# Kernel optimization log

Measured on AMD Instinct MI355X. Metric: run time of the kernel, lower is better.

Reference implementation:

```python
import jax, jax.numpy as jnp
import numpy as np

SEQ, D, N = 8192, 1024, 4096

def setup_inputs() -> dict:
    key = jax.random.key(0)
    kx, kw, kb = jax.random.split(key, 3)
    x = jax.random.normal(kx, (SEQ, D), dtype=jnp.float32)
    W = jax.random.normal(kw, (N, D), dtype=jnp.float32) * (1.0 / np.sqrt(D))
    b = jax.random.normal(kb, (N,), dtype=jnp.float32) * 0.01
    return {"x": x, "W": W, "b": b}

def reference(x, W, b):
    # Each NEURON computes tanh(w . e + b_i); stacking over neurons and
    # over the embedding list is a single fused matmul + bias + activation.
    # out: [seq, numNeurons]
    return jnp.tanh(jnp.einsum('sd,nd->sn', x, W) + b)
```

## Files before the change

kernel.cpp:

```cpp
#include <hip/hip_runtime.h>
#include <hip/hip_fp16.h>

#define SEQ 8192
#define DIM 1024
#define NN  4096
#define NT  16
#define A_BYTES ((size_t)SEQ * DIM * 2)
#define B_BYTES ((size_t)NN * DIM * 2)

using f16x8 = __attribute__((ext_vector_type(8))) _Float16;
using f16x4 = __attribute__((ext_vector_type(4))) _Float16;
using f32x4 = __attribute__((ext_vector_type(4))) float;

typedef __attribute__((address_space(1))) unsigned char as1_u8;
typedef __attribute__((address_space(3))) unsigned char as3_u8;

__device__ __forceinline__ float fast_tanh(float x) {
    float e = __expf(2.0f * x);
    return 1.0f - 2.0f / (e + 1.0f);
}

__global__ __launch_bounds__(256) void convert_kernel(
        const float* __restrict__ x, const float* __restrict__ w,
        f16x4* __restrict__ A, f16x4* __restrict__ B) {
    const int tid = threadIdx.x;
    const int b   = blockIdx.x;
    if (b < 8192) {
        const int gid = b * 256 + tid;
        const int s   = gid >> 8;
        const int c   = gid & 255;
        const float4 v = ((const float4*)x)[(size_t)s * 256 + c];
        const float f[4] = {v.x, v.y, v.z, v.w};
        f16x4 hv;
#pragma unroll
        for (int e = 0; e < 4; e++) hv[e] = (_Float16)f[e];
        A[(size_t)s * 256 + c] = hv;
    } else {
        const int gid = (b - 8192) * 256 + tid;
        const int n   = gid >> 8;
        const int c   = gid & 255;
        const float4 v = ((const float4*)w)[(size_t)n * 256 + c];
        const float f[4] = {v.x, v.y, v.z, v.w};
        f16x4 hv;
#pragma unroll
        for (int e = 0; e < 4; e++) hv[e] = (_Float16)f[e];
        B[(size_t)n * 256 + c] = hv;
    }
}

__global__ __launch_bounds__(512, 1) void gemm_tanh_kernel(
        const _Float16* __restrict__ A,
        const _Float16* __restrict__ B,
        const float* __restrict__ bias,
        float* __restrict__ out) {
    __shared__ _Float16 lds[65536];

    const int tid  = threadIdx.x;
    const int lane = tid & 63;
    const int wave = tid >> 6;
    const int wm   = wave >> 2;
    const int wn   = wave & 3;
    const int l15  = lane & 15;
    const int lq   = lane >> 4;

    const int wgid = ((blockIdx.x & 7) << 6) | (blockIdx.x >> 3);
    const int qb = wgid >> 5;
    const int pb = wgid & 31;
    const int rowBase = pb << 8;
    const int colBase = qb << 8;

    const int sw  = l15 & 7;
    const int gk0 = ((lq)     ^ sw) << 4;
    const int gk1 = ((4 + lq) ^ sw) << 4;
    const int aOff = wm * 2048 + l15 * 128;
    const int bOff = 32768 + wn * 2048 + l15 * 128;

    const int srow = tid >> 3;
    const int sg   = (tid & 7) ^ (srow & 7);
    const unsigned ldsWave = (unsigned)wave << 10;

    const _Float16* Ag = A + (size_t)(rowBase + srow) * DIM + sg * 8;
    const _Float16* Bg = B + (size_t)(colBase + srow) * DIM + sg * 8;
    char* ldsc = (char*)lds;

    auto stageA = [&](int kt, int h, int d) {
        const _Float16* g = Ag + (size_t)h * 128 * DIM + kt * 64;
        const unsigned lo = (unsigned)d * 65536u + (unsigned)h * 16384u + ldsWave;
        __builtin_amdgcn_global_load_lds((const as1_u8*)g,
                                         (as3_u8*)(ldsc + lo), 16, 0, 0);
        __builtin_amdgcn_global_load_lds((const as1_u8*)(g + (size_t)64 * DIM),
                                         (as3_u8*)(ldsc + lo + 8192), 16, 0, 0);
    };
    auto stageB = [&](int kt, int h, int d) {
        const _Float16* g = Bg + (size_t)h * 128 * DIM + kt * 64;
        const unsigned lo = (unsigned)d * 65536u + 32768u + (unsigned)h * 16384u + ldsWave;
        __builtin_amdgcn_global_load_lds((const as1_u8*)g,
                                         (as3_u8*)(ldsc + lo), 16, 0, 0);
        __builtin_amdgcn_global_load_lds((const as1_u8*)(g + (size_t)64 * DIM),
                                         (as3_u8*)(ldsc + lo + 8192), 16, 0, 0);
    };

    f32x4 acc[8][4] = {};
    f16x8 aH0[4][2], aH1[4][2], bN01[2][2], bN23[2][2];

    stageA(0, 0, 0); stageA(0, 1, 0); stageB(0, 0, 0); stageB(0, 1, 0);
    asm volatile("s_waitcnt vmcnt(0)" ::: "memory");
    __builtin_amdgcn_sched_barrier(0);
    __builtin_amdgcn_s_barrier();
    __builtin_amdgcn_sched_barrier(0);
#pragma unroll
    for (int i = 0; i < 4; ++i) {
        aH0[i][0] = *(const f16x8*)(ldsc + aOff + i * 4096 + gk0);
        aH0[i][1] = *(const f16x8*)(ldsc + aOff + i * 4096 + gk1);
    }
#pragma unroll
    for (int j = 0; j < 2; ++j) {
        bN01[j][0] = *(const f16x8*)(ldsc + bOff + j * 8192 + gk0);
        bN01[j][1] = *(const f16x8*)(ldsc + bOff + j * 8192 + gk1);
    }

    for (int t = 0; t < NT; ++t) {
        const int d  = t & 1;
        const int dn = d ^ 1;
        const char* lb  = ldsc + d * 65536;
        const char* lbn = ldsc + dn * 65536;

        if (t + 1 < NT) {
            stageA(t + 1, 0, dn); stageA(t + 1, 1, dn);
            stageB(t + 1, 0, dn); stageB(t + 1, 1, dn);
        }

#pragma unroll
        for (int j = 0; j < 2; ++j) {
            bN23[j][0] = *(const f16x8*)(lb + bOff + 16384 + j * 8192 + gk0);
            bN23[j][1] = *(const f16x8*)(lb + bOff + 16384 + j * 8192 + gk1);
        }
        __builtin_amdgcn_s_setprio(1);
#pragma unroll
        for (int k = 0; k < 2; ++k)
#pragma unroll
            for (int i = 0; i < 4; ++i)
#pragma unroll
                for (int j = 0; j < 2; ++j)
                    acc[i][j] = __builtin_amdgcn_mfma_f32_16x16x32_f16(
                        aH0[i][k], bN01[j][k], acc[i][j], 0, 0, 0);
        __builtin_amdgcn_s_setprio(0);

#pragma unroll
        for (int i = 0; i < 4; ++i) {
            aH1[i][0] = *(const f16x8*)(lb + aOff + 16384 + i * 4096 + gk0);
            aH1[i][1] = *(const f16x8*)(lb + aOff + 16384 + i * 4096 + gk1);
        }
        __builtin_amdgcn_s_setprio(1);
#pragma unroll
        for (int k = 0; k < 2; ++k)
#pragma unroll
            for (int i = 0; i < 4; ++i)
#pragma unroll
                for (int j = 0; j < 2; ++j)
                    acc[i][2 + j] = __builtin_amdgcn_mfma_f32_16x16x32_f16(
                        aH0[i][k], bN23[j][k], acc[i][2 + j], 0, 0, 0);
        __builtin_amdgcn_s_setprio(0);

        asm volatile("s_waitcnt lgkmcnt(0)" ::: "memory");
        __builtin_amdgcn_sched_barrier(0);
        asm volatile("s_waitcnt vmcnt(0)" ::: "memory");
        __builtin_amdgcn_sched_barrier(0);
        __builtin_amdgcn_s_barrier();
        __builtin_amdgcn_sched_barrier(0);

        if (t + 1 < NT) {
#pragma unroll
            for (int i = 0; i < 4; ++i) {
                aH0[i][0] = *(const f16x8*)(lbn + aOff + i * 4096 + gk0);
                aH0[i][1] = *(const f16x8*)(lbn + aOff + i * 4096 + gk1);
            }
        }
        __builtin_amdgcn_s_setprio(1);
#pragma unroll
        for (int k = 0; k < 2; ++k)
#pragma unroll
            for (int i = 0; i < 4; ++i)
#pragma unroll
                for (int j = 0; j < 2; ++j)
                    acc[4 + i][j] = __builtin_amdgcn_mfma_f32_16x16x32_f16(
                        aH1[i][k], bN01[j][k], acc[4 + i][j], 0, 0, 0);
        __builtin_amdgcn_s_setprio(0);

        if (t + 1 < NT) {
#pragma unroll
            for (int j = 0; j < 2; ++j) {
                bN01[j][0] = *(const f16x8*)(lbn + bOff + j * 8192 + gk0);
                bN01[j][1] = *(const f16x8*)(lbn + bOff + j * 8192 + gk1);
            }
        }
        __builtin_amdgcn_s_setprio(1);
#pragma unroll
        for (int k = 0; k < 2; ++k)
#pragma unroll
            for (int i = 0; i < 4; ++i)
#pragma unroll
                for (int j = 0; j < 2; ++j)
                    acc[4 + i][2 + j] = __builtin_amdgcn_mfma_f32_16x16x32_f16(
                        aH1[i][k], bN23[j][k], acc[4 + i][2 + j], 0, 0, 0);
        __builtin_amdgcn_s_setprio(0);
    }

#pragma unroll
    for (int j = 0; j < 4; ++j) {
        const int col = colBase + (j * 4 + wn) * 16 + l15;
        const float bj = bias[col];
#pragma unroll
        for (int r = 0; r < 8; ++r) {
            const size_t rb = (size_t)(rowBase + (r * 2 + wm) * 16 + lq * 4) * NN + col;
#pragma unroll
            for (int v = 0; v < 4; ++v)
                out[rb + (size_t)v * NN] = fast_tanh(acc[r][j][v] + bj);
        }
    }
}

__global__ void naive_gemm_kernel(const float* __restrict__ x,
                                  const float* __restrict__ W,
                                  const float* __restrict__ b,
                                  float* __restrict__ out) {
    __shared__ float xs[16][17], ws[16][17];
    int n = blockIdx.x * 16 + threadIdx.x;
    int m = blockIdx.y * 16 + threadIdx.y;
    float s = 0.f;
    for (int k0 = 0; k0 < DIM; k0 += 16) {
        xs[threadIdx.y][threadIdx.x] = x[(size_t)m * DIM + k0 + threadIdx.x];
        ws[threadIdx.y][threadIdx.x] =
            W[(size_t)(blockIdx.x * 16 + threadIdx.y) * DIM + k0 + threadIdx.x];
        __syncthreads();
#pragma unroll
        for (int kk = 0; kk < 16; kk++) s += xs[threadIdx.y][kk] * ws[threadIdx.x][kk];
        __syncthreads();
    }
    out[(size_t)m * NN + n] = tanhf(s + b[n]);
}

extern "C" void kernel_launch(void* const* d_in, const int* in_sizes, int n_in,
                              void* d_out, int out_size, void* d_ws, size_t ws_size,
                              hipStream_t stream) {
    const float* x = (const float*)d_in[0];
    const float* W = (const float*)d_in[1];
    const float* b = (const float*)d_in[2];
    float* out = (float*)d_out;

    const size_t need = A_BYTES + B_BYTES;
    if (ws_size < need) {
        dim3 grid(NN / 16, SEQ / 16), block(16, 16);
        naive_gemm_kernel<<<grid, block, 0, stream>>>(x, W, b, out);
        return;
    }

    _Float16* Abuf = (_Float16*)d_ws;
    _Float16* Bbuf = Abuf + (size_t)SEQ * DIM;

    convert_kernel<<<12288, 256, 0, stream>>>(x, W, (f16x4*)Abuf, (f16x4*)Bbuf);

    gemm_tanh_kernel<<<512, 512, 0, stream>>>(Abuf, Bbuf, b, out);
}
```

Measured before the change: 229.3 us.

## Use 4 waves per block with 128x128 per-wave tiles in GEMM

The block shrinks from 8 waves to 4. Each wave now computes a 128x128 output subtile (8x8 MFMA tiles) instead of 128x64, which gives more register-level reuse of A and B fragments per LDS read. Staging is rewritten so each thread issues 16 global_load_lds ops per k-tile, and the s_setprio hints are dropped. The cost is half the waves available to hide latency and a doubled accumulator footprint (256 VGPRs of accumulators), which risks spills or lower overlap.

```diff
diff --git a/kernel.cpp b/kernel.cpp
--- a/kernel.cpp
+++ b/kernel.cpp
@@ -48,7 +48,7 @@
     }
 }
 
-__global__ __launch_bounds__(512, 1) void gemm_tanh_kernel(
+__global__ __launch_bounds__(256, 1) void gemm_tanh_kernel(
         const _Float16* __restrict__ A,
         const _Float16* __restrict__ B,
         const float* __restrict__ bias,
@@ -58,8 +58,8 @@
     const int tid  = threadIdx.x;
     const int lane = tid & 63;
     const int wave = tid >> 6;
-    const int wm   = wave >> 2;
-    const int wn   = wave & 3;
+    const int wr   = wave >> 1;
+    const int wc   = wave & 1;
     const int l15  = lane & 15;
     const int lq   = lane >> 4;
 
@@ -72,95 +72,88 @@
     const int sw  = l15 & 7;
     const int gk0 = ((lq)     ^ sw) << 4;
     const int gk1 = ((4 + lq) ^ sw) << 4;
-    const int aOff = wm * 2048 + l15 * 128;
-    const int bOff = 32768 + wn * 2048 + l15 * 128;
+    const int aBase = wr * 16384 + l15 * 128;
+    const int bBase = 32768 + wc * 16384 + l15 * 128;
 
     const int srow = tid >> 3;
     const int sg   = (tid & 7) ^ (srow & 7);
-    const unsigned ldsWave = (unsigned)wave << 10;
-
     const _Float16* Ag = A + (size_t)(rowBase + srow) * DIM + sg * 8;
     const _Float16* Bg = B + (size_t)(colBase + srow) * DIM + sg * 8;
     char* ldsc = (char*)lds;
 
-    auto stageA = [&](int kt, int h, int d) {
-        const _Float16* g = Ag + (size_t)h * 128 * DIM + kt * 64;
-        const unsigned lo = (unsigned)d * 65536u + (unsigned)h * 16384u + ldsWave;
-        __builtin_amdgcn_global_load_lds((const as1_u8*)g,
-                                         (as3_u8*)(ldsc + lo), 16, 0, 0);
-        __builtin_amdgcn_global_load_lds((const as1_u8*)(g + (size_t)64 * DIM),
-                                         (as3_u8*)(ldsc + lo + 8192), 16, 0, 0);
+    auto stage = [&](int kt, int d) {
+        const unsigned db = (unsigned)d * 65536u + (unsigned)wave * 1024u;
+        const _Float16* ga = Ag + kt * 64;
+        const _Float16* gb = Bg + kt * 64;
+#pragma unroll
+        for (int h = 0; h < 2; ++h)
+#pragma unroll
+            for (int p = 0; p < 4; ++p)
+                __builtin_amdgcn_global_load_lds(
+                    (const as1_u8*)(ga + (size_t)(h * 128 + p * 32) * DIM),
+                    (as3_u8*)(ldsc + db + h * 16384u + p * 4096u), 16, 0, 0);
+#pragma unroll
+        for (int h = 0; h < 2; ++h)
+#pragma unroll
+            for (int p = 0; p < 4; ++p)
+                __builtin_amdgcn_global_load_lds(
+                    (const as1_u8*)(gb + (size_t)(h * 128 + p * 32) * DIM),
+                    (as3_u8*)(ldsc + db + 32768u + h * 16384u + p * 4096u), 16, 0, 0);
     };
-    auto stageB = [&](int kt, int h, int d) {
-        const _Float16* g = Bg + (size_t)h * 128 * DIM + kt * 64;
-        const unsigned lo = (unsigned)d * 65536u + 32768u + (unsigned)h * 16384u + ldsWave;
-        __builtin_amdgcn_global_load_lds((const as1_u8*)g,
-                                         (as3_u8*)(ldsc + lo), 16, 0, 0);
-        __builtin_amdgcn_global_load_lds((const as1_u8*)(g + (size_t)64 * DIM),
-                                         (as3_u8*)(ldsc + lo + 8192), 16, 0, 0);
+
+    f32x4 acc[8][8] = {};
+    f16x8 aH0[4][2], aH1[4][2], bN0[4][2], bN1[4][2];
+
+    auto readA = [&](f16x8 (&dst)[4][2], int half, int d) {
+        const char* p = ldsc + d * 65536 + aBase + half * 8192;
+#pragma unroll
+        for (int m = 0; m < 4; ++m) {
+            dst[m][0] = *(const f16x8*)(p + m * 2048 + gk0);
+            dst[m][1] = *(const f16x8*)(p + m * 2048 + gk1);
+        }
     };
-
-    f32x4 acc[8][4] = {};
-    f16x8 aH0[4][2], aH1[4][2], bN01[2][2], bN23[2][2];
-
-    stageA(0, 0, 0); stageA(0, 1, 0); stageB(0, 0, 0); stageB(0, 1, 0);
+    auto readB = [&](f16x8 (&dst)[4][2], int half, int d) {
+        const char* p = ldsc + d * 65536 + bBase + half * 8192;
+#pragma unroll
+        for (int n = 0; n < 4; ++n) {
+            dst[n][0] = *(const f16x8*)(p + n * 2048 + gk0);
+            dst[n][1] = *(const f16x8*)(p + n * 2048 + gk1);
+        }
+    };
+
+    stage(0, 0);
     asm volatile("s_waitcnt vmcnt(0)" ::: "memory");
     __builtin_amdgcn_sched_barrier(0);
     __builtin_amdgcn_s_barrier();
     __builtin_amdgcn_sched_barrier(0);
-#pragma unroll
-    for (int i = 0; i < 4; ++i) {
-        aH0[i][0] = *(const f16x8*)(ldsc + aOff + i * 4096 + gk0);
-        aH0[i][1] = *(const f16x8*)(ldsc + aOff + i * 4096 + gk1);
-    }
-#pragma unroll
-    for (int j = 0; j < 2; ++j) {
-        bN01[j][0] = *(const f16x8*)(ldsc + bOff + j * 8192 + gk0);
-        bN01[j][1] = *(const f16x8*)(ldsc + bOff + j * 8192 + gk1);
-    }
+    readA(aH0, 0, 0);
+    readB(bN0, 0, 0);
 
     for (int t = 0; t < NT; ++t) {
         const int d  = t & 1;
         const int dn = d ^ 1;
-        const char* lb  = ldsc + d * 65536;
-        const char* lbn = ldsc + dn * 65536;
-
-        if (t + 1 < NT) {
-            stageA(t + 1, 0, dn); stageA(t + 1, 1, dn);
-            stageB(t + 1, 0, dn); stageB(t + 1, 1, dn);
-        }
-
-#pragma unroll
-        for (int j = 0; j < 2; ++j) {
-            bN23[j][0] = *(const f16x8*)(lb + bOff + 16384 + j * 8192 + gk0);
-            bN23[j][1] = *(const f16x8*)(lb + bOff + 16384 + j * 8192 + gk1);
-        }
-        __builtin_amdgcn_s_setprio(1);
-#pragma unroll
-        for (int k = 0; k < 2; ++k)
-#pragma unroll
-            for (int i = 0; i < 4; ++i)
-#pragma unroll
-                for (int j = 0; j < 2; ++j)
+
+        if (t + 1 < NT) stage(t + 1, dn);
+
+        readB(bN1, 1, d);
+#pragma unroll
+        for (int k = 0; k < 2; ++k)
+#pragma unroll
+            for (int i = 0; i < 4; ++i)
+#pragma unroll
+                for (int j = 0; j < 4; ++j)
                     acc[i][j] = __builtin_amdgcn_mfma_f32_16x16x32_f16(
-                        aH0[i][k], bN01[j][k], acc[i][j], 0, 0, 0);
-        __builtin_amdgcn_s_setprio(0);
-
-#pragma unroll
-        for (int i = 0; i < 4; ++i) {
-            aH1[i][0] = *(const f16x8*)(lb + aOff + 16384 + i * 4096 + gk0);
-            aH1[i][1] = *(const f16x8*)(lb + aOff + 16384 + i * 4096 + gk1);
-        }
-        __builtin_amdgcn_s_setprio(1);
-#pragma unroll
-        for (int k = 0; k < 2; ++k)
-#pragma unroll
-            for (int i = 0; i < 4; ++i)
-#pragma unroll
-                for (int j = 0; j < 2; ++j)
-                    acc[i][2 + j] = __builtin_amdgcn_mfma_f32_16x16x32_f16(
-                        aH0[i][k], bN23[j][k], acc[i][2 + j], 0, 0, 0);
-        __builtin_amdgcn_s_setprio(0);
+                        aH0[i][k], bN0[j][k], acc[i][j], 0, 0, 0);
+
+        readA(aH1, 1, d);
+#pragma unroll
+        for (int k = 0; k < 2; ++k)
+#pragma unroll
+            for (int i = 0; i < 4; ++i)
+#pragma unroll
+                for (int j = 0; j < 4; ++j)
+                    acc[i][4 + j] = __builtin_amdgcn_mfma_f32_16x16x32_f16(
+                        aH0[i][k], bN1[j][k], acc[i][4 + j], 0, 0, 0);
 
         asm volatile("s_waitcnt lgkmcnt(0)" ::: "memory");
         __builtin_amdgcn_sched_barrier(0);
@@ -169,53 +162,37 @@
         __builtin_amdgcn_s_barrier();
         __builtin_amdgcn_sched_barrier(0);
 
-        if (t + 1 < NT) {
-#pragma unroll
-            for (int i = 0; i < 4; ++i) {
-                aH0[i][0] = *(const f16x8*)(lbn + aOff + i * 4096 + gk0);
-                aH0[i][1] = *(const f16x8*)(lbn + aOff + i * 4096 + gk1);
-            }
-        }
-        __builtin_amdgcn_s_setprio(1);
-#pragma unroll
-        for (int k = 0; k < 2; ++k)
-#pragma unroll
-            for (int i = 0; i < 4; ++i)
-#pragma unroll
-                for (int j = 0; j < 2; ++j)
+        if (t + 1 < NT) readA(aH0, 0, dn);
+#pragma unroll
+        for (int k = 0; k < 2; ++k)
+#pragma unroll
+            for (int i = 0; i < 4; ++i)
+#pragma unroll
+                for (int j = 0; j < 4; ++j)
                     acc[4 + i][j] = __builtin_amdgcn_mfma_f32_16x16x32_f16(
-                        aH1[i][k], bN01[j][k], acc[4 + i][j], 0, 0, 0);
-        __builtin_amdgcn_s_setprio(0);
-
-        if (t + 1 < NT) {
-#pragma unroll
-            for (int j = 0; j < 2; ++j) {
-                bN01[j][0] = *(const f16x8*)(lbn + bOff + j * 8192 + gk0);
-                bN01[j][1] = *(const f16x8*)(lbn + bOff + j * 8192 + gk1);
-            }
-        }
-        __builtin_amdgcn_s_setprio(1);
-#pragma unroll
-        for (int k = 0; k < 2; ++k)
-#pragma unroll
-            for (int i = 0; i < 4; ++i)
-#pragma unroll
-                for (int j = 0; j < 2; ++j)
-                    acc[4 + i][2 + j] = __builtin_amdgcn_mfma_f32_16x16x32_f16(
-                        aH1[i][k], bN23[j][k], acc[4 + i][2 + j], 0, 0, 0);
-        __builtin_amdgcn_s_setprio(0);
-    }
-
-#pragma unroll
-    for (int j = 0; j < 4; ++j) {
-        const int col = colBase + (j * 4 + wn) * 16 + l15;
+                        aH1[i][k], bN0[j][k], acc[4 + i][j], 0, 0, 0);
+
+        if (t + 1 < NT) readB(bN0, 0, dn);
+#pragma unroll
+        for (int k = 0; k < 2; ++k)
+#pragma unroll
+            for (int i = 0; i < 4; ++i)
+#pragma unroll
+                for (int j = 0; j < 4; ++j)
+                    acc[4 + i][4 + j] = __builtin_amdgcn_mfma_f32_16x16x32_f16(
+                        aH1[i][k], bN1[j][k], acc[4 + i][4 + j], 0, 0, 0);
+    }
+
+#pragma unroll
+    for (int n = 0; n < 8; ++n) {
+        const int col = colBase + wc * 128 + n * 16 + l15;
         const float bj = bias[col];
 #pragma unroll
-        for (int r = 0; r < 8; ++r) {
-            const size_t rb = (size_t)(rowBase + (r * 2 + wm) * 16 + lq * 4) * NN + col;
+        for (int m = 0; m < 8; ++m) {
+            const size_t rb = (size_t)(rowBase + wr * 128 + m * 16 + lq * 4) * NN + col;
 #pragma unroll
             for (int v = 0; v < 4; ++v)
-                out[rb + (size_t)v * NN] = fast_tanh(acc[r][j][v] + bj);
+                out[rb + (size_t)v * NN] = fast_tanh(acc[m][n][v] + bj);
         }
     }
 }
@@ -260,5 +237,5 @@
 
     convert_kernel<<<12288, 256, 0, stream>>>(x, W, (f16x4*)Abuf, (f16x4*)Bbuf);
 
-    gemm_tanh_kernel<<<512, 512, 0, stream>>>(Abuf, Bbuf, b, out);
-}
+    gemm_tanh_kernel<<<512, 256, 0, stream>>>(Abuf, Bbuf, b, out);
+}
```

New measurement: 250.5 us. 9.2% more time.
